# Kernel optimization log

Hardware: AMD Instinct MI355X
Metric: run time of the kernel (lower is better)

## Reference

```python
import jax, jax.numpy as jnp
import numpy as np

EMBED_DIM = 1024
NUM_HEADS = 16
HEAD_DIM = EMBED_DIM // NUM_HEADS
SEQ_LEN = 2048
BATCH = 2
THETA_BASE = 10000.0


def rope_angles(head_dim, max_seq_len):
    inv_freq = 1.0 / (THETA_BASE ** (jnp.arange(0, head_dim, 2, dtype=jnp.float32) / head_dim))
    pos = jnp.arange(max_seq_len, dtype=jnp.float32)
    angles = pos[:, None] * inv_freq[None, :]              # [S, D/2]
    angles = jnp.concatenate([angles, angles], axis=-1)    # [S, D]
    return jnp.cos(angles), jnp.sin(angles)


def apply_rope(x, cos, sin):
    # x: [B, H, S, D]; cos/sin: [S, D]
    d = x.shape[-1]
    x1, x2 = x[..., : d // 2], x[..., d // 2 :]
    rotated = jnp.concatenate([-x2, x1], axis=-1)
    return x * cos[None, None, :, :] + rotated * sin[None, None, :, :]


def setup_inputs() -> dict:
    key = jax.random.key(0)
    kx, kq, kk, kv, ko = jax.random.split(key, 5)
    s = 1.0 / np.sqrt(EMBED_DIM)
    return {
        "x": jax.random.normal(kx, (BATCH, SEQ_LEN, EMBED_DIM), dtype=jnp.float32),
        "Wq": jax.random.normal(kq, (EMBED_DIM, EMBED_DIM), dtype=jnp.float32) * s,
        "Wk": jax.random.normal(kk, (EMBED_DIM, EMBED_DIM), dtype=jnp.float32) * s,
        "Wv": jax.random.normal(kv, (EMBED_DIM, EMBED_DIM), dtype=jnp.float32) * s,
        "Wo": jax.random.normal(ko, (EMBED_DIM, EMBED_DIM), dtype=jnp.float32) * s,
    }


def reference(x, Wq, Wk, Wv, Wo):
    B, S, E = x.shape
    H, D = NUM_HEADS, HEAD_DIM
    cos, sin = rope_angles(D, S)

    def split_heads(t):
        return t.reshape(B, S, H, D).transpose(0, 2, 1, 3)  # [B,H,S,D]

    q = split_heads(x @ Wq.T)
    k = split_heads(x @ Wk.T)
    v = split_heads(x @ Wv.T)

    q = apply_rope(q, cos, sin)
    k = apply_rope(k, cos, sin)

    scores = jnp.einsum("bhsd,bhtd->bhst", q, k)
    causal = jnp.triu(jnp.ones((S, S), dtype=bool), k=1)
    scores = jnp.where(causal[None, None, :, :], -jnp.inf, scores)
    weights = jax.nn.softmax(scores / jnp.sqrt(jnp.float32(D)), axis=-1)

    ctx = jnp.einsum("bhst,bhtd->bhsd", weights, v)
    ctx = ctx.transpose(0, 2, 1, 3).reshape(B, S, E)
    return ctx @ Wo.T
```

## Files before the change

### kernel.cpp

```cpp
#include <hip/hip_runtime.h>
#include <hip/hip_bf16.h>

#define H_NUM 16
#define D_DIM 64
#define S_LEN 2048
#define EMB   1024
#define M_TOT 4096

typedef unsigned short u16;
typedef unsigned int   u32;
typedef __attribute__((ext_vector_type(8))) short short8;
typedef __attribute__((ext_vector_type(4))) float f32x4;

__device__ __forceinline__ u32 f2bf_u(float f) {
    u32 u = __float_as_uint(f);
    return (u + 0x7fffu + ((u >> 16) & 1u)) >> 16;
}
__device__ __forceinline__ u32 pack2(float a, float b) {
    return f2bf_u(a) | (f2bf_u(b) << 16);
}
__device__ __forceinline__ u32 pack2t(float a, float b) {
    return __builtin_amdgcn_perm(__float_as_uint(b), __float_as_uint(a),
                                 0x07060302u);
}
__device__ __forceinline__ uint4 pack8(float4 lo, float4 hi) {
    return make_uint4(pack2(lo.x, lo.y), pack2(lo.z, lo.w),
                      pack2(hi.x, hi.y), pack2(hi.z, hi.w));
}

__device__ __forceinline__ void lds_dma16(const u16* g, u16* l) {
    __builtin_amdgcn_global_load_lds(
        (const __attribute__((address_space(1))) void*)g,
        (__attribute__((address_space(3))) void*)l, 16, 0, 0);
}

__global__ __launch_bounds__(256) void cast_kernel(
    const float* __restrict__ x,  const float* __restrict__ Wq,
    const float* __restrict__ Wk, const float* __restrict__ Wv,
    const float* __restrict__ Wo, u16* __restrict__ ws, float2* __restrict__ tab)
{
    const int seg = blockIdx.y;
    if (seg == 5) {
        const int idx = blockIdx.x * 256 + threadIdx.x;
        if (idx < S_LEN * 32) {
            const int s = idx >> 5, d = idx & 31;
            const float ang = (float)s * __expf(-(float)d * 0.28782313662425573f);
            tab[idx] = make_float2(cosf(ang), sinf(ang));
        }
        return;
    }
    const float* src = (seg == 0) ? x : (seg == 1) ? Wq : (seg == 2) ? Wk
                     : (seg == 3) ? Wv : Wo;
    u16* dst = (seg == 0) ? ws : ws + (3 + seg) * 1048576;
    const int n = (seg == 0) ? 4194304 : 1048576;
    const int idx = (blockIdx.x * 256 + threadIdx.x) * 8;
    if (idx < n) {
        float4 lo = *(const float4*)(src + idx);
        float4 hi = *(const float4*)(src + idx + 4);
        *(uint4*)(dst + idx) = pack8(lo, hi);
    }
}

__global__ __launch_bounds__(256) void qkv_rope_kernel(
    const u16* __restrict__ xb, const u16* __restrict__ wb,
    const float2* __restrict__ tab,
    u16* __restrict__ qo, u16* __restrict__ ko, u16* __restrict__ vo)
{
    const int w  = blockIdx.y >> 3;
    const int nb = blockIdx.y & 7;
    const u16* W = wb + w * 1048576;

    __shared__ __align__(16) u16 smem[12288];
    u16* As = smem;
    u16* Bs = smem + 64 * 64;
    u16 (*Ep)[132] = (u16(*)[132])smem;

    const int tid   = threadIdx.x;
    const int lane  = tid & 63;
    const int wid   = tid >> 6;
    const int waveM = wid >> 1;
    const int waveN = wid & 1;
    const int col16 = lane & 15;
    const int quad  = lane >> 4;

    const int m0 = blockIdx.x * 64;
    const int n0 = nb * 128;

    f32x4 acc[2][4];
    const f32x4 zero4 = {0.f, 0.f, 0.f, 0.f};
#pragma unroll
    for (int i = 0; i < 2; i++)
#pragma unroll
        for (int j = 0; j < 4; j++) acc[i][j] = zero4;

    const int drow = tid >> 3;
    const int dpos = tid & 7;
    const u16* Ag = xb + (size_t)m0 * EMB;
    const u16* Bg = W  + (size_t)n0 * EMB;

    for (int k0 = 0; k0 < EMB; k0 += 64) {
        __syncthreads();
#pragma unroll
        for (int j = 0; j < 2; j++) {
            const int rl = j * 32 + drow;
            const int cg = dpos ^ (rl & 7);
            lds_dma16(Ag + (size_t)rl * EMB + k0 + cg * 8,
                      As + (j * 32 + wid * 8) * 64);
        }
#pragma unroll
        for (int j = 0; j < 4; j++) {
            const int rl = j * 32 + drow;
            const int cg = dpos ^ (rl & 7);
            lds_dma16(Bg + (size_t)rl * EMB + k0 + cg * 8,
                      Bs + (j * 32 + wid * 8) * 64);
        }
        __syncthreads();

        short8 af[2][2], bf[4][2];
#pragma unroll
        for (int mt = 0; mt < 2; mt++) {
            const int r = waveM * 32 + mt * 16 + col16;
#pragma unroll
            for (int ks = 0; ks < 2; ks++) {
                const int p = (ks * 4 + quad) ^ (r & 7);
                af[mt][ks] = *(const short8*)(As + r * 64 + p * 8);
            }
        }
#pragma unroll
        for (int nt = 0; nt < 4; nt++) {
            const int r = waveN * 64 + nt * 16 + col16;
#pragma unroll
            for (int ks = 0; ks < 2; ks++) {
                const int p = (ks * 4 + quad) ^ (r & 7);
                bf[nt][ks] = *(const short8*)(Bs + r * 64 + p * 8);
            }
        }
#pragma unroll
        for (int ks = 0; ks < 2; ks++)
#pragma unroll
            for (int mt = 0; mt < 2; mt++)
#pragma unroll
                for (int nt = 0; nt < 4; nt++)
                    acc[mt][nt] = __builtin_amdgcn_mfma_f32_16x16x32_bf16(
                        af[mt][ks], bf[nt][ks], acc[mt][nt], 0, 0, 0);
    }

    const float qs = (w == 0) ? 0.18033688011112042f : 1.0f;
    __syncthreads();
#pragma unroll
    for (int mt = 0; mt < 2; mt++) {
#pragma unroll
        for (int r = 0; r < 4; r++) {
            const int m_local = waveM * 32 + mt * 16 + quad * 4 + r;
            const int s = (m0 + m_local) & 2047;
            if (w == 2) {
#pragma unroll
                for (int nt = 0; nt < 4; nt++)
                    Ep[m_local][waveN * 64 + nt * 16 + col16] =
                        (u16)f2bf_u(acc[mt][nt][r]);
            } else {
#pragma unroll
                for (int nt = 0; nt < 2; nt++) {
                    const int d = nt * 16 + col16;
                    const float2 cs = tab[s * 32 + d];
                    const float lo = acc[mt][nt][r];
                    const float hi = acc[mt][nt + 2][r];
                    Ep[m_local][waveN * 64 + d]      =
                        (u16)f2bf_u((lo * cs.x - hi * cs.y) * qs);
                    Ep[m_local][waveN * 64 + d + 32] =
                        (u16)f2bf_u((hi * cs.x + lo * cs.y) * qs);
                }
            }
        }
    }
    __syncthreads();

    const int b = m0 >> 11;
    if (w != 2) {
        u16* out = (w == 0) ? qo : ko;
#pragma unroll
        for (int j = 0; j < 4; j++) {
            const int g = j * 256 + tid;
            const int head_local = g >> 9;
            const int sl  = (g >> 3) & 63;
            const int cir = g & 7;
            uint4 val = *(const uint4*)(&Ep[sl][head_local * 64 + cir * 8]);
            const int h = (n0 >> 6) + head_local;
            const size_t base = (((size_t)(b * H_NUM + h)) * S_LEN + (m0 & 2047)) * 64;
            *(uint4*)(out + base + (size_t)(g & 511) * 8) = val;
        }
    } else {
        const int s0 = m0 & 2047;
#pragma unroll
        for (int j = 0; j < 4; j++) {
            const int g = j * 256 + tid;
            const int d_all = g >> 3;
            const int sc = g & 7;
            u32 wv[4];
#pragma unroll
            for (int hw = 0; hw < 4; hw++) {
                const int p0 = sc * 8 + hw * 2;
                const int r0 = ((p0 & 3) << 4) | (p0 >> 2);
                const int p1 = p0 + 1;
                const int r1 = ((p1 & 3) << 4) | (p1 >> 2);
                wv[hw] = (u32)Ep[r0][d_all] | ((u32)Ep[r1][d_all] << 16);
            }
            const int h = (n0 >> 6) + (d_all >> 6);
            const int d = d_all & 63;
            *(uint4*)(vo + ((size_t)(b * H_NUM + h) * 64 + d) * 2048 + s0 + sc * 8) =
                make_uint4(wv[0], wv[1], wv[2], wv[3]);
        }
    }
}

__global__ __launch_bounds__(512, 4) void attn_kernel(
    const u16* __restrict__ q, const u16* __restrict__ k,
    const u16* __restrict__ v, u16* __restrict__ ctx)
{
    __shared__ __align__(16) u16 QP[2][64 * 64];
    __shared__ __align__(16) u16 Ks[2][2][64 * 64];
    __shared__ __align__(16) u16 VTs[2][2][64 * 64];

    const int tid   = threadIdx.x;
    const int lane  = tid & 63;
    const int wid   = tid >> 6;
    const int w4    = wid & 3;
    const int g     = wid >> 2;
    const int col16 = lane & 15;
    const int quad  = lane >> 4;

    const int bh = blockIdx.x;
    const int p  = blockIdx.y;
    const int qbA = p;
    const int qbB = 31 - p;
    const int qBaseA = qbA * 64;
    const int qBaseB = qbB * 64;
    const size_t bhOff = (size_t)bh * S_LEN * D_DIM;

    const int srow = tid >> 3;
    const int spos = tid & 7;
    const int scg  = spos ^ (srow & 7);

    auto stage = [&](int kt, int buf, int slot) {
        lds_dma16(k + bhOff + (size_t)(kt * 64 + srow) * 64 + scg * 8,
                  &Ks[buf][slot][wid * 512]);
        lds_dma16(v + bhOff + (size_t)srow * 2048 + kt * 64 + scg * 8,
                  &VTs[buf][slot][wid * 512]);
    };

    stage(0, 0, 0);
    stage(1, 0, 1);
    {
        const int stBase = g ? qBaseB : qBaseA;
        const int r5 = srow & 31;
#pragma unroll
        for (int j = 0; j < 2; j++) {
            const int rl = j * 32 + r5;
            const int cg = spos ^ (rl & 7);
            lds_dma16(q + bhOff + (size_t)(stBase + rl) * 64 + cg * 8,
                      QP[g] + (j * 32 + w4 * 8) * 64);
        }
    }
    __syncthreads();

    short8 qfA[2], qfB[2];
    {
        const int rq = w4 * 16 + col16;
#pragma unroll
        for (int ks = 0; ks < 2; ks++) {
            const int c = (ks * 4 + quad) ^ (rq & 7);
            qfA[ks] = *(const short8*)(QP[0] + rq * 64 + c * 8);
            qfB[ks] = *(const short8*)(QP[1] + rq * 64 + c * 8);
        }
    }

    u16* myP = ((u16*)QP) + wid * 1024;

    const short ONE = (short)0x3F80;
    const short8 onesf = {ONE, ONE, ONE, ONE, ONE, ONE, ONE, ONE};

    f32x4 OA[4], OB[4];
    const f32x4 zero4 = {0.f, 0.f, 0.f, 0.f};
#pragma unroll
    for (int j = 0; j < 4; j++) { OA[j] = zero4; OB[j] = zero4; }
    f32x4 laccA = zero4, laccB = zero4;

    auto proc = [&](const short8* qf, f32x4* O, f32x4& lacc,
                    int qBase, int qb, int kt, int bufv) {
        const int sl = g;
        f32x4 sc[4];
#pragma unroll
        for (int nt = 0; nt < 4; nt++) sc[nt] = zero4;
#pragma unroll
        for (int ks = 0; ks < 2; ks++) {
            short8 kf[4];
#pragma unroll
            for (int nt = 0; nt < 4; nt++) {
                const int rk = nt * 16 + col16;
                const int c = (ks * 4 + quad) ^ (rk & 7);
                kf[nt] = *(const short8*)(&Ks[bufv][sl][rk * 64 + c * 8]);
            }
            __builtin_amdgcn_s_setprio(1);
#pragma unroll
            for (int nt = 0; nt < 4; nt++)
                sc[nt] = __builtin_amdgcn_mfma_f32_16x16x32_bf16(
                    qf[ks], kf[nt], sc[nt], 0, 0, 0);
            __builtin_amdgcn_s_setprio(0);
        }

        if (kt == qb) {
#pragma unroll
            for (int r = 0; r < 4; r++) {
                const int qg = qBase + w4 * 16 + quad * 4 + r;
#pragma unroll
                for (int nt = 0; nt < 4; nt++) {
                    const int kg = kt * 64 + nt * 16 + col16;
                    float pv = __builtin_amdgcn_exp2f(sc[nt][r]);
                    if (kg > qg) pv = 0.f;
                    sc[nt][r] = pv;
                }
            }
        } else {
#pragma unroll
            for (int r = 0; r < 4; r++)
#pragma unroll
                for (int nt = 0; nt < 4; nt++)
                    sc[nt][r] = __builtin_amdgcn_exp2f(sc[nt][r]);
        }

#pragma unroll
        for (int r = 0; r < 4; r++) {
            const int ml = quad * 4 + r;
            const u32 lo = pack2t(sc[0][r], sc[1][r]);
            const u32 hi = pack2t(sc[2][r], sc[3][r]);
            *(uint2*)(myP + ml * 64 +
                      (((col16 >> 1) ^ (ml & 7)) * 8 + (col16 & 1) * 4)) =
                make_uint2(lo, hi);
        }

#pragma unroll
        for (int ks = 0; ks < 2; ks++) {
            short8 pf, vf[4];
            {
                const int c = (ks * 4 + quad) ^ (col16 & 7);
                pf = *(const short8*)(myP + col16 * 64 + c * 8);
            }
#pragma unroll
            for (int dt = 0; dt < 4; dt++) {
                const int d = dt * 16 + col16;
                const int c = (ks * 4 + quad) ^ (d & 7);
                vf[dt] = *(const short8*)(&VTs[bufv][sl][d * 64 + c * 8]);
            }
            __builtin_amdgcn_s_setprio(1);
#pragma unroll
            for (int dt = 0; dt < 4; dt++)
                O[dt] = __builtin_amdgcn_mfma_f32_16x16x32_bf16(
                    pf, vf[dt], O[dt], 0, 0, 0);
            lacc = __builtin_amdgcn_mfma_f32_16x16x32_bf16(
                pf, onesf, lacc, 0, 0, 0);
            __builtin_amdgcn_s_setprio(0);
        }
    };

    int buf = 0;
    for (int kt0 = 0; kt0 <= qbB; kt0 += 2) {
        __syncthreads();
        if (kt0 + 2 <= qbB) {
            stage(kt0 + 2, buf ^ 1, 0);
            if (kt0 + 3 <= qbB) stage(kt0 + 3, buf ^ 1, 1);
        }
        const int kt = kt0 + g;
        if (kt <= qbB) {
            proc(qfB, OB, laccB, qBaseB, qbB, kt, buf);
            if (kt <= qbA)
                proc(qfA, OA, laccA, qBaseA, qbA, kt, buf);
        }
        buf ^= 1;
    }

    __syncthreads();
    {
        float* eb = (g ? (float*)&VTs[0][0][0] : (float*)&Ks[0][0][0])
                    + w4 * 1296;
        f32x4* eO = g ? OA : OB;
        f32x4  eL = g ? laccA : laccB;
#pragma unroll
        for (int dt = 0; dt < 4; dt++)
            *(f32x4*)(eb + lane * 20 + dt * 4) = eO[dt];
        if (col16 == 0)
            *(f32x4*)(eb + 1280 + quad * 4) = eL;
    }
    __syncthreads();
    f32x4 myO[4];
    f32x4 myL;
    {
        float* ib = (g ? (float*)&Ks[0][0][0] : (float*)&VTs[0][0][0])
                    + w4 * 1296;
#pragma unroll
        for (int dt = 0; dt < 4; dt++) {
            const f32x4 pp = *(const f32x4*)(ib + lane * 20 + dt * 4);
            myO[dt] = (g ? OB[dt] : OA[dt]) + pp;
        }
        const f32x4 lp = *(const f32x4*)(ib + 1280 + quad * 4);
        myL = (g ? laccB : laccA) + lp;
    }

    const int b = bh >> 4, h = bh & 15;
    const int outBase = g ? qBaseB : qBaseA;
#pragma unroll
    for (int r = 0; r < 4; r++) {
        const int ml = quad * 4 + r;
        const float inv = __builtin_amdgcn_rcpf(myL[r]);
        const u32 lo = pack2t(myO[0][r] * inv, myO[1][r] * inv);
        const u32 hi = pack2t(myO[2][r] * inv, myO[3][r] * inv);
        *(uint2*)(myP + ml * 64 +
                  (((col16 >> 1) ^ (ml & 7)) * 8 + (col16 & 1) * 4)) =
            make_uint2(lo, hi);
    }
#pragma unroll
    for (int j = 0; j < 2; j++) {
        const int gg  = j * 64 + lane;
        const int sl = gg >> 3;
        const int cir = gg & 7;
        u32 wv[4];
#pragma unroll
        for (int hw = 0; hw < 4; hw++) {
            const int d0 = cir * 8 + hw * 2;
            const int p0 = ((d0 & 15) << 2) | (d0 >> 4);
            const int d1 = d0 + 1;
            const int p1 = ((d1 & 15) << 2) | (d1 >> 4);
            const u16 v0 = myP[sl * 64 + ((p0 >> 3) ^ (sl & 7)) * 8 + (p0 & 7)];
            const u16 v1 = myP[sl * 64 + ((p1 >> 3) ^ (sl & 7)) * 8 + (p1 & 7)];
            wv[hw] = (u32)v0 | ((u32)v1 << 16);
        }
        const size_t rowbase =
            ((size_t)b * S_LEN + outBase + w4 * 16 + sl) * EMB + h * 64;
        *(uint4*)(ctx + rowbase + cir * 8) = make_uint4(wv[0], wv[1], wv[2], wv[3]);
    }
}

__global__ __launch_bounds__(256) void proj_kernel(
    const u16* __restrict__ X, const u16* __restrict__ W, float* __restrict__ out)
{
    __shared__ __align__(16) u16 smem[16384];

    const int tid   = threadIdx.x;
    const int lane  = tid & 63;
    const int wid   = tid >> 6;
    const int col16 = lane & 15;
    const int quad  = lane >> 4;

    const int m0 = blockIdx.x * 64;
    const int n0 = blockIdx.y * 64;

    u16* As = smem;
    u16* Bs = smem + 64 * 128;

    f32x4 acc[4];
    const f32x4 zero4 = {0.f, 0.f, 0.f, 0.f};
#pragma unroll
    for (int i = 0; i < 4; i++) acc[i] = zero4;

    const int srow4 = lane >> 4;
    const int pos   = lane & 15;
    const u16* Ag = X + (size_t)m0 * EMB;
    const u16* Bg = W + (size_t)n0 * EMB;

    for (int kk = 0; kk < 8; kk++) {
        const int k0 = kk * 128;
        __syncthreads();
#pragma unroll
        for (int jj = 0; jj < 4; jj++) {
            const int row = jj * 16 + wid * 4 + srow4;
            const int cg = (pos & 8) | ((pos & 7) ^ (row & 7));
            lds_dma16(Ag + (size_t)row * EMB + k0 + cg * 8,
                      As + (jj * 16 + wid * 4) * 128);
        }
#pragma unroll
        for (int jj = 0; jj < 4; jj++) {
            const int row = jj * 16 + wid * 4 + srow4;
            const int cg = (pos & 8) | ((pos & 7) ^ (row & 7));
            lds_dma16(Bg + (size_t)row * EMB + k0 + cg * 8,
                      Bs + (jj * 16 + wid * 4) * 128);
        }
        __syncthreads();

#pragma unroll
        for (int half = 0; half < 2; half++) {
            short8 af[2], bf[4][2];
            {
                const int r = wid * 16 + col16;
#pragma unroll
                for (int ks = 0; ks < 2; ks++) {
                    const int p = half * 8 + (((ks * 4 + quad)) ^ (r & 7));
                    af[ks] = *(const short8*)(As + r * 128 + p * 8);
                }
            }
#pragma unroll
            for (int nt = 0; nt < 4; nt++) {
                const int r = nt * 16 + col16;
#pragma unroll
                for (int ks = 0; ks < 2; ks++) {
                    const int p = half * 8 + (((ks * 4 + quad)) ^ (r & 7));
                    bf[nt][ks] = *(const short8*)(Bs + r * 128 + p * 8);
                }
            }
#pragma unroll
            for (int ks = 0; ks < 2; ks++)
#pragma unroll
                for (int nt = 0; nt < 4; nt++)
                    acc[nt] = __builtin_amdgcn_mfma_f32_16x16x32_bf16(
                        bf[nt][ks], af[ks], acc[nt], 0, 0, 0);
        }
    }

#pragma unroll
    for (int nt = 0; nt < 4; nt++) {
        const int m_g = m0 + wid * 16 + col16;
        const int n_g = n0 + nt * 16 + quad * 4;
        *(f32x4*)(out + (size_t)m_g * EMB + n_g) = acc[nt];
    }
}

extern "C" void kernel_launch(void* const* d_in, const int* in_sizes, int n_in,
                              void* d_out, int out_size, void* d_ws, size_t ws_size,
                              hipStream_t stream)
{
    const float* x  = (const float*)d_in[0];
    const float* Wq = (const float*)d_in[1];
    const float* Wk = (const float*)d_in[2];
    const float* Wv = (const float*)d_in[3];
    const float* Wo = (const float*)d_in[4];

    u16* ws = (u16*)d_ws;
    u16* xb  = ws;
    u16* wb  = ws + 4194304;
    u16* wob = ws + 7340032;
    u16* q   = ws + 8388608;
    u16* k   = ws + 12582912;
    u16* v   = ws + 16777216;
    u16* ctx = ws + 20971520;
    float2* tab = (float2*)(ws + 25165824);

    cast_kernel<<<dim3(2048, 6), 256, 0, stream>>>(x, Wq, Wk, Wv, Wo, ws, tab);
    qkv_rope_kernel<<<dim3(64, 24), 256, 0, stream>>>(xb, wb, tab, q, k, v);
    attn_kernel<<<dim3(32, 16), 512, 0, stream>>>(q, k, v, ctx);
    proj_kernel<<<dim3(64, 16), 256, 0, stream>>>(ctx, wob, (float*)d_out);
}
```

Measured before the change: 158.8 us.

## Share weight tile across two M sub-tiles in 512-thread QKV GEMM blocks

The QKV+RoPE GEMM block grows from 256 to 512 threads and covers 128 rows of M instead of 64. Two groups of four waves each use their own A tile but read the same 128-column B tile from LDS. This halves the global loads of the weight tile per output row and halves the grid. In exchange the kernel uses more LDS per block and launches fewer, larger blocks, which may lower occupancy and wave-level parallelism.

```diff
diff --git a/kernel.cpp b/kernel.cpp
--- a/kernel.cpp
+++ b/kernel.cpp
@@ -61,7 +61,7 @@
     }
 }
 
-__global__ __launch_bounds__(256) void qkv_rope_kernel(
+__global__ __launch_bounds__(512) void qkv_rope_kernel(
     const u16* __restrict__ xb, const u16* __restrict__ wb,
     const float2* __restrict__ tab,
     u16* __restrict__ qo, u16* __restrict__ ko, u16* __restrict__ vo)
@@ -70,20 +70,22 @@
     const int nb = blockIdx.y & 7;
     const u16* W = wb + w * 1048576;
 
-    __shared__ __align__(16) u16 smem[12288];
-    u16* As = smem;
-    u16* Bs = smem + 64 * 64;
-    u16 (*Ep)[132] = (u16(*)[132])smem;
+    __shared__ __align__(16) u16 smem[16896];
+    u16* As0 = smem;
+    u16* As1 = smem + 4096;
+    u16* Bs  = smem + 8192;
 
     const int tid   = threadIdx.x;
     const int lane  = tid & 63;
     const int wid   = tid >> 6;
-    const int waveM = wid >> 1;
-    const int waveN = wid & 1;
+    const int t     = wid >> 2;
+    const int sub   = wid & 3;
+    const int waveM = sub >> 1;
+    const int waveN = sub & 1;
     const int col16 = lane & 15;
     const int quad  = lane >> 4;
 
-    const int m0 = blockIdx.x * 64;
+    const int m0 = blockIdx.x * 128;
     const int n0 = nb * 128;
 
     f32x4 acc[2][4];
@@ -93,26 +95,26 @@
 #pragma unroll
         for (int j = 0; j < 4; j++) acc[i][j] = zero4;
 
-    const int drow = tid >> 3;
-    const int dpos = tid & 7;
+    const int srow = tid >> 3;
+    const int spos = tid & 7;
+    const int scg  = spos ^ (srow & 7);
     const u16* Ag = xb + (size_t)m0 * EMB;
     const u16* Bg = W  + (size_t)n0 * EMB;
+    u16* myAs = t ? As1 : As0;
 
     for (int k0 = 0; k0 < EMB; k0 += 64) {
         __syncthreads();
+        lds_dma16(Ag + (size_t)srow * EMB + k0 + scg * 8, As0 + wid * 512);
+        lds_dma16(Ag + (size_t)(64 + srow) * EMB + k0 + scg * 8,
+                  As1 + wid * 512);
 #pragma unroll
         for (int j = 0; j < 2; j++) {
-            const int rl = j * 32 + drow;
-            const int cg = dpos ^ (rl & 7);
-            lds_dma16(Ag + (size_t)rl * EMB + k0 + cg * 8,
-                      As + (j * 32 + wid * 8) * 64);
-        }
-#pragma unroll
-        for (int j = 0; j < 4; j++) {
-            const int rl = j * 32 + drow;
-            const int cg = dpos ^ (rl & 7);
-            lds_dma16(Bg + (size_t)rl * EMB + k0 + cg * 8,
-                      Bs + (j * 32 + wid * 8) * 64);
+            const int c = j * 512 + tid;
+            const int row = c >> 3;
+            const int pos = c & 7;
+            const int cg = pos ^ (row & 7);
+            lds_dma16(Bg + (size_t)row * EMB + k0 + cg * 8,
+                      Bs + j * 4096 + wid * 512);
         }
         __syncthreads();
 
@@ -123,7 +125,7 @@
 #pragma unroll
             for (int ks = 0; ks < 2; ks++) {
                 const int p = (ks * 4 + quad) ^ (r & 7);
-                af[mt][ks] = *(const short8*)(As + r * 64 + p * 8);
+                af[mt][ks] = *(const short8*)(myAs + r * 64 + p * 8);
             }
         }
 #pragma unroll
@@ -147,12 +149,13 @@
 
     const float qs = (w == 0) ? 0.18033688011112042f : 1.0f;
     __syncthreads();
+    u16 (*Ep)[132] = (u16(*)[132])(smem + t * 8448);
 #pragma unroll
     for (int mt = 0; mt < 2; mt++) {
 #pragma unroll
         for (int r = 0; r < 4; r++) {
             const int m_local = waveM * 32 + mt * 16 + quad * 4 + r;
-            const int s = (m0 + m_local) & 2047;
+            const int s = (m0 + t * 64 + m_local) & 2047;
             if (w == 2) {
 #pragma unroll
                 for (int nt = 0; nt < 4; nt++)
@@ -175,25 +178,27 @@
     }
     __syncthreads();
 
-    const int b = m0 >> 11;
+    const int tid2 = tid & 255;
+    const int bt = (m0 + t * 64) >> 11;
     if (w != 2) {
         u16* out = (w == 0) ? qo : ko;
+        const int sBase = (m0 + t * 64) & 2047;
 #pragma unroll
         for (int j = 0; j < 4; j++) {
-            const int g = j * 256 + tid;
+            const int g = j * 256 + tid2;
             const int head_local = g >> 9;
             const int sl  = (g >> 3) & 63;
             const int cir = g & 7;
             uint4 val = *(const uint4*)(&Ep[sl][head_local * 64 + cir * 8]);
             const int h = (n0 >> 6) + head_local;
-            const size_t base = (((size_t)(b * H_NUM + h)) * S_LEN + (m0 & 2047)) * 64;
+            const size_t base = (((size_t)(bt * H_NUM + h)) * S_LEN + sBase) * 64;
             *(uint4*)(out + base + (size_t)(g & 511) * 8) = val;
         }
     } else {
-        const int s0 = m0 & 2047;
+        const int s0 = (m0 + t * 64) & 2047;
 #pragma unroll
         for (int j = 0; j < 4; j++) {
-            const int g = j * 256 + tid;
+            const int g = j * 256 + tid2;
             const int d_all = g >> 3;
             const int sc = g & 7;
             u32 wv[4];
@@ -207,7 +212,7 @@
             }
             const int h = (n0 >> 6) + (d_all >> 6);
             const int d = d_all & 63;
-            *(uint4*)(vo + ((size_t)(b * H_NUM + h) * 64 + d) * 2048 + s0 + sc * 8) =
+            *(uint4*)(vo + ((size_t)(bt * H_NUM + h) * 64 + d) * 2048 + s0 + sc * 8) =
                 make_uint4(wv[0], wv[1], wv[2], wv[3]);
         }
     }
@@ -543,7 +548,7 @@
     float2* tab = (float2*)(ws + 25165824);
 
     cast_kernel<<<dim3(2048, 6), 256, 0, stream>>>(x, Wq, Wk, Wv, Wo, ws, tab);
-    qkv_rope_kernel<<<dim3(64, 24), 256, 0, stream>>>(xb, wb, tab, q, k, v);
+    qkv_rope_kernel<<<dim3(32, 24), 512, 0, stream>>>(xb, wb, tab, q, k, v);
     attn_kernel<<<dim3(32, 16), 512, 0, stream>>>(q, k, v, ctx);
     proj_kernel<<<dim3(64, 16), 256, 0, stream>>>(ctx, wob, (float*)d_out);
 }
```

New measurement: 163.7 us. +3.1%, slower.
